# Performance work log

Hardware: AMD Instinct MI355X
Metric: run time of the kernel (lower is better)

## Reference

```python
import jax, jax.numpy as jnp
import numpy as np

N = 50000   # nodes
E = 600000  # directed edges (avg degree ~12)
F_IN = 128
HID = 128
N_LAYERS = 7


def setup_inputs() -> dict:
    key = jax.random.key(0)
    ks = jax.random.split(key, 5)
    x = jax.random.normal(ks[0], (N, F_IN), dtype=jnp.float32)
    edge_index = jax.random.randint(ks[1], (2, E), 0, N, dtype=jnp.int64)
    Ws = jax.random.normal(ks[2], (N_LAYERS, F_IN, HID), dtype=jnp.float32) * 0.05
    bs = jnp.zeros((N_LAYERS, HID), dtype=jnp.float32)
    lin_w = jax.random.normal(ks[3], (HID, 1), dtype=jnp.float32) * 0.05
    lin_b = jnp.zeros((1,), dtype=jnp.float32)
    return {"x": x, "edge_index": edge_index, "Ws": Ws, "bs": bs,
            "lin_w": lin_w, "lin_b": lin_b}


def reference(x, edge_index, Ws, bs, lin_w, lin_b):
    n = x.shape[0]
    loop = jnp.arange(n, dtype=edge_index.dtype)
    # PyG GCNConv default: add self-loops, symmetric normalization.
    src = jnp.concatenate([edge_index[0], loop])  # [E+N] message sources (j)
    dst = jnp.concatenate([edge_index[1], loop])  # [E+N] message targets (i)
    deg = jax.ops.segment_sum(jnp.ones_like(dst, dtype=x.dtype), dst, num_segments=n)
    dis = jnp.where(deg > 0, jax.lax.rsqrt(deg), 0.0)  # deg^-1/2, 0 for isolated
    norm = dis[src] * dis[dst]                          # [E+N]

    def gcn_layer(h, W, b):
        h = h @ W                                        # linear first (as in PyG)
        msg = h[src] * norm[:, None]                     # gather + scale
        return jax.ops.segment_sum(msg, dst, num_segments=n) + b

    h = x
    for i in range(N_LAYERS):
        h = jax.nn.relu(gcn_layer(h, Ws[i], bs[i]))
    out = h @ lin_w + lin_b                              # [N, 1]
    return out.squeeze()                                 # [N]
```

## Files before the change

### kernel.cpp

```cpp
#include <hip/hip_runtime.h>

#define HID 128
#define ASPITCH 132
#define BM 64


__global__ __launch_bounds__(256) void k_count(const int* __restrict__ ei, int E,
                                               int* __restrict__ deg) {
    int e = blockIdx.x * 256 + threadIdx.x;
    if (e < E) atomicAdd(&deg[ei[E + e]], 1);
}

__global__ __launch_bounds__(256) void k_scan1(const int* __restrict__ deg,
                                               int* __restrict__ rowptr,
                                               int* __restrict__ partial, int n) {
    __shared__ int s[256];
    int tid = threadIdx.x;
    int i = blockIdx.x * 256 + tid;
    int v = (i < n) ? deg[i] : 0;
    s[tid] = v;
    __syncthreads();
    for (int off = 1; off < 256; off <<= 1) {
        int t = (tid >= off) ? s[tid - off] : 0;
        __syncthreads();
        s[tid] += t;
        __syncthreads();
    }
    if (i < n) rowptr[i] = s[tid] - v;
    if (tid == 255) partial[blockIdx.x] = s[255];
}

__global__ __launch_bounds__(256) void k_scan2(int* __restrict__ partial, int nb) {
    __shared__ int s[256];
    int tid = threadIdx.x;
    int v = (tid < nb) ? partial[tid] : 0;
    s[tid] = v;
    __syncthreads();
    for (int off = 1; off < 256; off <<= 1) {
        int t = (tid >= off) ? s[tid - off] : 0;
        __syncthreads();
        s[tid] += t;
        __syncthreads();
    }
    if (tid < nb) partial[tid] = s[tid] - v;
}

__global__ __launch_bounds__(256) void k_scan3(int* __restrict__ rowptr,
                                               const int* __restrict__ partial,
                                               int n, int E) {
    int i = blockIdx.x * 256 + threadIdx.x;
    if (i < n) rowptr[i] += partial[blockIdx.x];
    if (i == 0) rowptr[n] = E;
}

__global__ __launch_bounds__(256) void k_dis(const int* __restrict__ deg,
                                             float* __restrict__ dis, int n) {
    int i = blockIdx.x * 256 + threadIdx.x;
    if (i < n) dis[i] = 1.0f / sqrtf((float)(deg[i] + 1));
}

__global__ __launch_bounds__(256) void k_fill(const int* __restrict__ ei, int E,
                                              const int* __restrict__ rowptr,
                                              int* __restrict__ cursor,
                                              int* __restrict__ col) {
    int e = blockIdx.x * 256 + threadIdx.x;
    if (e < E) {
        int d = ei[E + e];
        int p = atomicAdd(&cursor[d], 1);
        col[rowptr[d] + p] = ei[e];
    }
}


__global__ __launch_bounds__(256, 3) void k_gemm0(const float* __restrict__ A,
                                                  const float* __restrict__ W,
                                                  const float* __restrict__ dis,
                                                  float* __restrict__ T, int n) {
    __shared__ float As[BM * ASPITCH];
    int r0 = blockIdx.x * BM;
    int tid = threadIdx.x;
    int rows = n - r0; if (rows > BM) rows = BM;
    {
        const float4* A4 = (const float4*)(A + (size_t)r0 * HID);
        int tot = rows * (HID / 4);
        for (int i = tid; i < tot; i += 256) {
            int row = i >> 5, c = (i & 31) << 2;
            *(float4*)&As[row * ASPITCH + c] = A4[i];
        }
    }
    __syncthreads();

    int tx = tid & 31, ty = tid >> 5;
    int rr0 = ty * 8;
    const float4* W4 = (const float4*)W;

    float acc[8][4];
    #pragma unroll
    for (int r = 0; r < 8; ++r) { acc[r][0]=0.f; acc[r][1]=0.f; acc[r][2]=0.f; acc[r][3]=0.f; }

    float4 wa0 = W4[0 * 32 + tx];
    float4 wa1 = W4[1 * 32 + tx];
    float4 wa2 = W4[2 * 32 + tx];
    float4 wa3 = W4[3 * 32 + tx];
    float4 wb0, wb1, wb2, wb3;

    #pragma unroll 1
    for (int k = 0; k < HID; k += 8) {
        wb0 = W4[(k + 4) * 32 + tx];
        wb1 = W4[(k + 5) * 32 + tx];
        wb2 = W4[(k + 6) * 32 + tx];
        wb3 = W4[(k + 7) * 32 + tx];
        #pragma unroll
        for (int r = 0; r < 8; ++r) {
            float4 a = *(const float4*)&As[(rr0 + r) * ASPITCH + k];
            acc[r][0] = fmaf(a.x, wa0.x, acc[r][0]);
            acc[r][1] = fmaf(a.x, wa0.y, acc[r][1]);
            acc[r][2] = fmaf(a.x, wa0.z, acc[r][2]);
            acc[r][3] = fmaf(a.x, wa0.w, acc[r][3]);
            acc[r][0] = fmaf(a.y, wa1.x, acc[r][0]);
            acc[r][1] = fmaf(a.y, wa1.y, acc[r][1]);
            acc[r][2] = fmaf(a.y, wa1.z, acc[r][2]);
            acc[r][3] = fmaf(a.y, wa1.w, acc[r][3]);
            acc[r][0] = fmaf(a.z, wa2.x, acc[r][0]);
            acc[r][1] = fmaf(a.z, wa2.y, acc[r][1]);
            acc[r][2] = fmaf(a.z, wa2.z, acc[r][2]);
            acc[r][3] = fmaf(a.z, wa2.w, acc[r][3]);
            acc[r][0] = fmaf(a.w, wa3.x, acc[r][0]);
            acc[r][1] = fmaf(a.w, wa3.y, acc[r][1]);
            acc[r][2] = fmaf(a.w, wa3.z, acc[r][2]);
            acc[r][3] = fmaf(a.w, wa3.w, acc[r][3]);
        }
        if (k + 8 < HID) {
            wa0 = W4[(k + 8)  * 32 + tx];
            wa1 = W4[(k + 9)  * 32 + tx];
            wa2 = W4[(k + 10) * 32 + tx];
            wa3 = W4[(k + 11) * 32 + tx];
        }
        #pragma unroll
        for (int r = 0; r < 8; ++r) {
            float4 a = *(const float4*)&As[(rr0 + r) * ASPITCH + k + 4];
            acc[r][0] = fmaf(a.x, wb0.x, acc[r][0]);
            acc[r][1] = fmaf(a.x, wb0.y, acc[r][1]);
            acc[r][2] = fmaf(a.x, wb0.z, acc[r][2]);
            acc[r][3] = fmaf(a.x, wb0.w, acc[r][3]);
            acc[r][0] = fmaf(a.y, wb1.x, acc[r][0]);
            acc[r][1] = fmaf(a.y, wb1.y, acc[r][1]);
            acc[r][2] = fmaf(a.y, wb1.z, acc[r][2]);
            acc[r][3] = fmaf(a.y, wb1.w, acc[r][3]);
            acc[r][0] = fmaf(a.z, wb2.x, acc[r][0]);
            acc[r][1] = fmaf(a.z, wb2.y, acc[r][1]);
            acc[r][2] = fmaf(a.z, wb2.z, acc[r][2]);
            acc[r][3] = fmaf(a.z, wb2.w, acc[r][3]);
            acc[r][0] = fmaf(a.w, wb3.x, acc[r][0]);
            acc[r][1] = fmaf(a.w, wb3.y, acc[r][1]);
            acc[r][2] = fmaf(a.w, wb3.z, acc[r][2]);
            acc[r][3] = fmaf(a.w, wb3.w, acc[r][3]);
        }
    }

    int c0 = tx * 4;
    #pragma unroll
    for (int r = 0; r < 8; ++r) {
        int row = rr0 + r;
        if (row < rows) {
            float d = dis[r0 + row];
            float4 o = make_float4(acc[r][0] * d, acc[r][1] * d, acc[r][2] * d, acc[r][3] * d);
            *(float4*)&T[(size_t)(r0 + row) * HID + c0] = o;
        }
    }
}

__global__ __launch_bounds__(256, 3) void k_aggemm(const float* __restrict__ Uin,
                                                   const float* __restrict__ W,
                                                   const float* __restrict__ b,
                                                   const float* __restrict__ dis,
                                                   const int* __restrict__ rowptr,
                                                   const int* __restrict__ col,
                                                   float* __restrict__ Uout, int n) {
    __shared__ float S[BM * HID];
    int r0 = blockIdx.x * BM;
    int tid = threadIdx.x;
    int hw = tid >> 5, lane = tid & 31;
    size_t foff = (size_t)(lane * 4);
    float4 bb = *(const float4*)&b[lane * 4];

    #pragma unroll 1
    for (int rr = 0; rr < 8; ++rr) {
        int row = r0 + hw * 8 + rr;
        float4 acc = make_float4(0.f, 0.f, 0.f, 0.f);
        if (row < n) {
            acc = *(const float4*)&Uin[(size_t)row * HID + foff];
            float4 acc2 = make_float4(0.f, 0.f, 0.f, 0.f);
            int e = rowptr[row], e1 = rowptr[row + 1];
            for (; e + 8 <= e1; e += 8) {
                int j0 = col[e + 0];
                int j1 = col[e + 1];
                int j2 = col[e + 2];
                int j3 = col[e + 3];
                int j4 = col[e + 4];
                int j5 = col[e + 5];
                int j6 = col[e + 6];
                int j7 = col[e + 7];
                float4 v0 = *(const float4*)&Uin[(size_t)j0 * HID + foff];
                float4 v1 = *(const float4*)&Uin[(size_t)j1 * HID + foff];
                float4 v2 = *(const float4*)&Uin[(size_t)j2 * HID + foff];
                float4 v3 = *(const float4*)&Uin[(size_t)j3 * HID + foff];
                float4 v4 = *(const float4*)&Uin[(size_t)j4 * HID + foff];
                float4 v5 = *(const float4*)&Uin[(size_t)j5 * HID + foff];
                float4 v6 = *(const float4*)&Uin[(size_t)j6 * HID + foff];
                float4 v7 = *(const float4*)&Uin[(size_t)j7 * HID + foff];
                acc.x  += (v0.x + v1.x) + (v2.x + v3.x);
                acc.y  += (v0.y + v1.y) + (v2.y + v3.y);
                acc.z  += (v0.z + v1.z) + (v2.z + v3.z);
                acc.w  += (v0.w + v1.w) + (v2.w + v3.w);
                acc2.x += (v4.x + v5.x) + (v6.x + v7.x);
                acc2.y += (v4.y + v5.y) + (v6.y + v7.y);
                acc2.z += (v4.z + v5.z) + (v6.z + v7.z);
                acc2.w += (v4.w + v5.w) + (v6.w + v7.w);
            }
            for (; e + 2 <= e1; e += 2) {
                int j0 = col[e + 0];
                int j1 = col[e + 1];
                float4 v0 = *(const float4*)&Uin[(size_t)j0 * HID + foff];
                float4 v1 = *(const float4*)&Uin[(size_t)j1 * HID + foff];
                acc.x  += v0.x; acc.y  += v0.y; acc.z  += v0.z; acc.w  += v0.w;
                acc2.x += v1.x; acc2.y += v1.y; acc2.z += v1.z; acc2.w += v1.w;
            }
            if (e < e1) {
                int j = col[e];
                float4 v = *(const float4*)&Uin[(size_t)j * HID + foff];
                acc.x += v.x; acc.y += v.y; acc.z += v.z; acc.w += v.w;
            }
            float d = dis[row];
            acc.x = fmaxf(fmaf(d, acc.x + acc2.x, bb.x), 0.0f);
            acc.y = fmaxf(fmaf(d, acc.y + acc2.y, bb.y), 0.0f);
            acc.z = fmaxf(fmaf(d, acc.z + acc2.z, bb.z), 0.0f);
            acc.w = fmaxf(fmaf(d, acc.w + acc2.w, bb.w), 0.0f);
        }
        *(float4*)&S[(hw * 8 + rr) * HID + lane * 4] = acc;
    }

    int tx = tid & 31, ty = tid >> 5;
    int rr0 = ty * 8;
    const float4* W4 = (const float4*)W;

    float acc[8][4];
    #pragma unroll
    for (int r = 0; r < 8; ++r) { acc[r][0]=0.f; acc[r][1]=0.f; acc[r][2]=0.f; acc[r][3]=0.f; }

    float4 wa0 = W4[0 * 32 + tx];
    float4 wa1 = W4[1 * 32 + tx];
    float4 wa2 = W4[2 * 32 + tx];
    float4 wa3 = W4[3 * 32 + tx];
    float4 wb0, wb1, wb2, wb3;

    #pragma unroll 1
    for (int k = 0; k < HID; k += 8) {
        wb0 = W4[(k + 4) * 32 + tx];
        wb1 = W4[(k + 5) * 32 + tx];
        wb2 = W4[(k + 6) * 32 + tx];
        wb3 = W4[(k + 7) * 32 + tx];
        #pragma unroll
        for (int r = 0; r < 8; ++r) {
            float4 a = *(const float4*)&S[(rr0 + r) * HID + k];
            acc[r][0] = fmaf(a.x, wa0.x, acc[r][0]);
            acc[r][1] = fmaf(a.x, wa0.y, acc[r][1]);
            acc[r][2] = fmaf(a.x, wa0.z, acc[r][2]);
            acc[r][3] = fmaf(a.x, wa0.w, acc[r][3]);
            acc[r][0] = fmaf(a.y, wa1.x, acc[r][0]);
            acc[r][1] = fmaf(a.y, wa1.y, acc[r][1]);
            acc[r][2] = fmaf(a.y, wa1.z, acc[r][2]);
            acc[r][3] = fmaf(a.y, wa1.w, acc[r][3]);
            acc[r][0] = fmaf(a.z, wa2.x, acc[r][0]);
            acc[r][1] = fmaf(a.z, wa2.y, acc[r][1]);
            acc[r][2] = fmaf(a.z, wa2.z, acc[r][2]);
            acc[r][3] = fmaf(a.z, wa2.w, acc[r][3]);
            acc[r][0] = fmaf(a.w, wa3.x, acc[r][0]);
            acc[r][1] = fmaf(a.w, wa3.y, acc[r][1]);
            acc[r][2] = fmaf(a.w, wa3.z, acc[r][2]);
            acc[r][3] = fmaf(a.w, wa3.w, acc[r][3]);
        }
        if (k + 8 < HID) {
            wa0 = W4[(k + 8)  * 32 + tx];
            wa1 = W4[(k + 9)  * 32 + tx];
            wa2 = W4[(k + 10) * 32 + tx];
            wa3 = W4[(k + 11) * 32 + tx];
        }
        #pragma unroll
        for (int r = 0; r < 8; ++r) {
            float4 a = *(const float4*)&S[(rr0 + r) * HID + k + 4];
            acc[r][0] = fmaf(a.x, wb0.x, acc[r][0]);
            acc[r][1] = fmaf(a.x, wb0.y, acc[r][1]);
            acc[r][2] = fmaf(a.x, wb0.z, acc[r][2]);
            acc[r][3] = fmaf(a.x, wb0.w, acc[r][3]);
            acc[r][0] = fmaf(a.y, wb1.x, acc[r][0]);
            acc[r][1] = fmaf(a.y, wb1.y, acc[r][1]);
            acc[r][2] = fmaf(a.y, wb1.z, acc[r][2]);
            acc[r][3] = fmaf(a.y, wb1.w, acc[r][3]);
            acc[r][0] = fmaf(a.z, wb2.x, acc[r][0]);
            acc[r][1] = fmaf(a.z, wb2.y, acc[r][1]);
            acc[r][2] = fmaf(a.z, wb2.z, acc[r][2]);
            acc[r][3] = fmaf(a.z, wb2.w, acc[r][3]);
            acc[r][0] = fmaf(a.w, wb3.x, acc[r][0]);
            acc[r][1] = fmaf(a.w, wb3.y, acc[r][1]);
            acc[r][2] = fmaf(a.w, wb3.z, acc[r][2]);
            acc[r][3] = fmaf(a.w, wb3.w, acc[r][3]);
        }
    }

    int rows = n - r0; if (rows > BM) rows = BM;
    int c0 = tx * 4;
    #pragma unroll
    for (int r = 0; r < 8; ++r) {
        int row = rr0 + r;
        if (row < rows) {
            float d = dis[r0 + row];
            float4 o = make_float4(acc[r][0] * d, acc[r][1] * d, acc[r][2] * d, acc[r][3] * d);
            *(float4*)&Uout[(size_t)(r0 + row) * HID + c0] = o;
        }
    }
}

__global__ __launch_bounds__(256) void k_agglin(const float* __restrict__ Uin,
                                                const float* __restrict__ b,
                                                const float* __restrict__ dis,
                                                const int* __restrict__ rowptr,
                                                const int* __restrict__ col,
                                                const float* __restrict__ lw,
                                                const float* __restrict__ lb,
                                                float* __restrict__ out, int n) {
    int node = (blockIdx.x * 256 + threadIdx.x) >> 5;
    int lane = threadIdx.x & 31;
    if (node >= n) return;
    size_t foff = (size_t)(lane * 4);
    float4 acc = *(const float4*)&Uin[(size_t)node * HID + foff];
    float4 acc2 = make_float4(0.f, 0.f, 0.f, 0.f);
    int e = rowptr[node], e1 = rowptr[node + 1];
    for (; e + 8 <= e1; e += 8) {
        int j0 = col[e + 0];
        int j1 = col[e + 1];
        int j2 = col[e + 2];
        int j3 = col[e + 3];
        int j4 = col[e + 4];
        int j5 = col[e + 5];
        int j6 = col[e + 6];
        int j7 = col[e + 7];
        float4 v0 = *(const float4*)&Uin[(size_t)j0 * HID + foff];
        float4 v1 = *(const float4*)&Uin[(size_t)j1 * HID + foff];
        float4 v2 = *(const float4*)&Uin[(size_t)j2 * HID + foff];
        float4 v3 = *(const float4*)&Uin[(size_t)j3 * HID + foff];
        float4 v4 = *(const float4*)&Uin[(size_t)j4 * HID + foff];
        float4 v5 = *(const float4*)&Uin[(size_t)j5 * HID + foff];
        float4 v6 = *(const float4*)&Uin[(size_t)j6 * HID + foff];
        float4 v7 = *(const float4*)&Uin[(size_t)j7 * HID + foff];
        acc.x  += (v0.x + v1.x) + (v2.x + v3.x);
        acc.y  += (v0.y + v1.y) + (v2.y + v3.y);
        acc.z  += (v0.z + v1.z) + (v2.z + v3.z);
        acc.w  += (v0.w + v1.w) + (v2.w + v3.w);
        acc2.x += (v4.x + v5.x) + (v6.x + v7.x);
        acc2.y += (v4.y + v5.y) + (v6.y + v7.y);
        acc2.z += (v4.z + v5.z) + (v6.z + v7.z);
        acc2.w += (v4.w + v5.w) + (v6.w + v7.w);
    }
    for (; e + 2 <= e1; e += 2) {
        int j0 = col[e + 0];
        int j1 = col[e + 1];
        float4 v0 = *(const float4*)&Uin[(size_t)j0 * HID + foff];
        float4 v1 = *(const float4*)&Uin[(size_t)j1 * HID + foff];
        acc.x  += v0.x; acc.y  += v0.y; acc.z  += v0.z; acc.w  += v0.w;
        acc2.x += v1.x; acc2.y += v1.y; acc2.z += v1.z; acc2.w += v1.w;
    }
    if (e < e1) {
        int j = col[e];
        float4 v = *(const float4*)&Uin[(size_t)j * HID + foff];
        acc.x += v.x; acc.y += v.y; acc.z += v.z; acc.w += v.w;
    }
    float d = dis[node];
    float4 bb = *(const float4*)&b[lane * 4];
    float4 h;
    h.x = fmaxf(fmaf(d, acc.x + acc2.x, bb.x), 0.0f);
    h.y = fmaxf(fmaf(d, acc.y + acc2.y, bb.y), 0.0f);
    h.z = fmaxf(fmaf(d, acc.z + acc2.z, bb.z), 0.0f);
    h.w = fmaxf(fmaf(d, acc.w + acc2.w, bb.w), 0.0f);
    float4 ww = *(const float4*)&lw[lane * 4];
    float s = h.x * ww.x + h.y * ww.y + h.z * ww.z + h.w * ww.w;
    #pragma unroll
    for (int o = 16; o > 0; o >>= 1) s += __shfl_down(s, o, 64);
    if (lane == 0) out[node] = s + lb[0];
}


extern "C" void kernel_launch(void* const* d_in, const int* in_sizes, int n_in,
                              void* d_out, int out_size, void* d_ws, size_t ws_size,
                              hipStream_t stream) {
    const float* x     = (const float*)d_in[0];
    const int*   ei    = (const int*)d_in[1];
    const float* Ws    = (const float*)d_in[2];
    const float* bs    = (const float*)d_in[3];
    const float* lin_w = (const float*)d_in[4];
    const float* lin_b = (const float*)d_in[5];
    float* out = (float*)d_out;

    int n = in_sizes[0] / HID;
    int E = in_sizes[1] / 2;
    int L = in_sizes[2] / (HID * HID);

    char* ws = (char*)d_ws;
    size_t off = 0;
    auto alloc = [&](size_t bytes) -> void* {
        void* p = ws + off;
        off += (bytes + 255) & ~(size_t)255;
        return p;
    };
    int*   deg     = (int*)alloc((size_t)n * 4);
    int*   cursor  = (int*)alloc((size_t)n * 4);
    int*   rowptr  = (int*)alloc((size_t)(n + 1) * 4);
    int*   partial = (int*)alloc(1024);
    float* dis     = (float*)alloc((size_t)n * 4);
    int*   col     = (int*)alloc((size_t)E * 4);
    float* ubuf0   = (float*)alloc((size_t)n * HID * 4);
    float* ubuf1   = (float*)alloc((size_t)n * HID * 4);
    (void)ws_size;

    hipMemsetAsync(deg, 0, (size_t)n * 4, stream);
    hipMemsetAsync(cursor, 0, (size_t)n * 4, stream);

    int eb = (E + 255) / 256;
    int nb = (n + 255) / 256;
    k_count<<<eb, 256, 0, stream>>>(ei, E, deg);
    k_scan1<<<nb, 256, 0, stream>>>(deg, rowptr, partial, n);
    k_scan2<<<1, 256, 0, stream>>>(partial, nb);
    k_scan3<<<nb, 256, 0, stream>>>(rowptr, partial, n, E);
    k_dis<<<nb, 256, 0, stream>>>(deg, dis, n);
    k_fill<<<eb, 256, 0, stream>>>(ei, E, rowptr, cursor, col);

    int gb = (n + BM - 1) / BM;
    int hb = (n + 7) / 8;

    k_gemm0<<<gb, 256, 0, stream>>>(x, Ws, dis, ubuf0, n);

    float* uin = ubuf0;
    float* uout = ubuf1;
    for (int i = 0; i + 1 < L; ++i) {
        k_aggemm<<<gb, 256, 0, stream>>>(uin, Ws + (size_t)(i + 1) * HID * HID,
                                         bs + (size_t)i * HID, dis, rowptr, col,
                                         uout, n);
        float* t = uin; uin = uout; uout = t;
    }

    k_agglin<<<hb, 256, 0, stream>>>(uin, bs + (size_t)(L - 1) * HID, dis,
                                     rowptr, col, lin_w, lin_b, out, n);
}
```

Baseline: 566.2 us.

## Remap aggregation so each wavefront gathers 16 rows in parallel with masked loop

The gather-aggregate phase of the fused aggregate+GEMM kernel now assigns 4 lanes per row, so each 64-lane wavefront handles 16 rows at once. It loops over 8 feature slices of 16 floats, instead of one row at a time across 32 lanes. Neighbor loops use a wave-uniform masked loop with 4 loads in flight, so rows of different degree share iterations. The aim is more independent memory requests in flight and better latency hiding for the random gathers. In exchange, each 16-byte access is less coalesced, and col/rowptr reads repeat across the 8 feature slices, with idle masked lanes when degrees differ.

```diff
diff --git a/kernel.cpp b/kernel.cpp
--- a/kernel.cpp
+++ b/kernel.cpp
@@ -180,64 +180,61 @@
     __shared__ float S[BM * HID];
     int r0 = blockIdx.x * BM;
     int tid = threadIdx.x;
-    int hw = tid >> 5, lane = tid & 31;
-    size_t foff = (size_t)(lane * 4);
-    float4 bb = *(const float4*)&b[lane * 4];
-
-    #pragma unroll 1
-    for (int rr = 0; rr < 8; ++rr) {
-        int row = r0 + hw * 8 + rr;
-        float4 acc = make_float4(0.f, 0.f, 0.f, 0.f);
-        if (row < n) {
-            acc = *(const float4*)&Uin[(size_t)row * HID + foff];
+
+    {
+        int w = tid >> 6;
+        int lane = tid & 63;
+        int rowslot = lane >> 2;
+        int flane = lane & 3;
+        int lrow = w * 16 + rowslot;
+        int row = r0 + lrow;
+        bool rv = row < n;
+        int e0 = 0, e1 = 0;
+        float dd = 0.f;
+        if (rv) { e0 = rowptr[row]; e1 = rowptr[row + 1]; dd = dis[row]; }
+
+        #pragma unroll 1
+        for (int s = 0; s < 8; ++s) {
+            int fo = s * 16 + flane * 4;
+            float4 bb = *(const float4*)&b[fo];
+            float4 acc = make_float4(0.f, 0.f, 0.f, 0.f);
             float4 acc2 = make_float4(0.f, 0.f, 0.f, 0.f);
-            int e = rowptr[row], e1 = rowptr[row + 1];
-            for (; e + 8 <= e1; e += 8) {
-                int j0 = col[e + 0];
-                int j1 = col[e + 1];
-                int j2 = col[e + 2];
-                int j3 = col[e + 3];
-                int j4 = col[e + 4];
-                int j5 = col[e + 5];
-                int j6 = col[e + 6];
-                int j7 = col[e + 7];
-                float4 v0 = *(const float4*)&Uin[(size_t)j0 * HID + foff];
-                float4 v1 = *(const float4*)&Uin[(size_t)j1 * HID + foff];
-                float4 v2 = *(const float4*)&Uin[(size_t)j2 * HID + foff];
-                float4 v3 = *(const float4*)&Uin[(size_t)j3 * HID + foff];
-                float4 v4 = *(const float4*)&Uin[(size_t)j4 * HID + foff];
-                float4 v5 = *(const float4*)&Uin[(size_t)j5 * HID + foff];
-                float4 v6 = *(const float4*)&Uin[(size_t)j6 * HID + foff];
-                float4 v7 = *(const float4*)&Uin[(size_t)j7 * HID + foff];
-                acc.x  += (v0.x + v1.x) + (v2.x + v3.x);
-                acc.y  += (v0.y + v1.y) + (v2.y + v3.y);
-                acc.z  += (v0.z + v1.z) + (v2.z + v3.z);
-                acc.w  += (v0.w + v1.w) + (v2.w + v3.w);
-                acc2.x += (v4.x + v5.x) + (v6.x + v7.x);
-                acc2.y += (v4.y + v5.y) + (v6.y + v7.y);
-                acc2.z += (v4.z + v5.z) + (v6.z + v7.z);
-                acc2.w += (v4.w + v5.w) + (v6.w + v7.w);
+            if (rv) acc = *(const float4*)&Uin[(size_t)row * HID + fo];
+            int e = e0;
+            while (__any(e < e1)) {
+                bool m0 = e + 0 < e1, m1 = e + 1 < e1, m2 = e + 2 < e1, m3 = e + 3 < e1;
+                int j0 = col[m0 ? e + 0 : 0];
+                int j1 = col[m1 ? e + 1 : 0];
+                int j2 = col[m2 ? e + 2 : 0];
+                int j3 = col[m3 ? e + 3 : 0];
+                float4 v0 = *(const float4*)&Uin[(size_t)j0 * HID + fo];
+                float4 v1 = *(const float4*)&Uin[(size_t)j1 * HID + fo];
+                float4 v2 = *(const float4*)&Uin[(size_t)j2 * HID + fo];
+                float4 v3 = *(const float4*)&Uin[(size_t)j3 * HID + fo];
+                float4 z = make_float4(0.f, 0.f, 0.f, 0.f);
+                float4 w0_ = m0 ? v0 : z;
+                float4 w1_ = m1 ? v1 : z;
+                float4 w2_ = m2 ? v2 : z;
+                float4 w3_ = m3 ? v3 : z;
+                acc.x  += w0_.x + w1_.x;
+                acc.y  += w0_.y + w1_.y;
+                acc.z  += w0_.z + w1_.z;
+                acc.w  += w0_.w + w1_.w;
+                acc2.x += w2_.x + w3_.x;
+                acc2.y += w2_.y + w3_.y;
+                acc2.z += w2_.z + w3_.z;
+                acc2.w += w2_.w + w3_.w;
+                e += 4;
             }
-            for (; e + 2 <= e1; e += 2) {
-                int j0 = col[e + 0];
-                int j1 = col[e + 1];
-                float4 v0 = *(const float4*)&Uin[(size_t)j0 * HID + foff];
-                float4 v1 = *(const float4*)&Uin[(size_t)j1 * HID + foff];
-                acc.x  += v0.x; acc.y  += v0.y; acc.z  += v0.z; acc.w  += v0.w;
-                acc2.x += v1.x; acc2.y += v1.y; acc2.z += v1.z; acc2.w += v1.w;
+            float4 h = make_float4(0.f, 0.f, 0.f, 0.f);
+            if (rv) {
+                h.x = fmaxf(fmaf(dd, acc.x + acc2.x, bb.x), 0.0f);
+                h.y = fmaxf(fmaf(dd, acc.y + acc2.y, bb.y), 0.0f);
+                h.z = fmaxf(fmaf(dd, acc.z + acc2.z, bb.z), 0.0f);
+                h.w = fmaxf(fmaf(dd, acc.w + acc2.w, bb.w), 0.0f);
             }
-            if (e < e1) {
-                int j = col[e];
-                float4 v = *(const float4*)&Uin[(size_t)j * HID + foff];
-                acc.x += v.x; acc.y += v.y; acc.z += v.z; acc.w += v.w;
-            }
-            float d = dis[row];
-            acc.x = fmaxf(fmaf(d, acc.x + acc2.x, bb.x), 0.0f);
-            acc.y = fmaxf(fmaf(d, acc.y + acc2.y, bb.y), 0.0f);
-            acc.z = fmaxf(fmaf(d, acc.z + acc2.z, bb.z), 0.0f);
-            acc.w = fmaxf(fmaf(d, acc.w + acc2.w, bb.w), 0.0f);
-        }
-        *(float4*)&S[(hw * 8 + rr) * HID + lane * 4] = acc;
+            *(float4*)&S[lrow * HID + fo] = h;
+        }
     }
 
     int tx = tid & 31, ty = tid >> 5;
```

Measured after the change: 670.1 us. +18.3%, slower.
